# Performance work log

Hardware: AMD Instinct MI355X
Metric: run time of the kernel (lower is better)

Reference implementation:

```python
import jax, jax.numpy as jnp
import numpy as np


def setup_inputs() -> dict:
    key = jax.random.key(0)
    ks = jax.random.split(key, 8)
    B, I, H = 4096, 2048, 2048
    C = I + H
    s = 1.0 / np.sqrt(C)
    return {
        "x": jax.random.normal(ks[0], (B, I), jnp.float32),
        "h": jax.random.normal(ks[1], (B, H), jnp.float32),
        "W_update": jax.random.normal(ks[2], (H, C), jnp.float32) * s,
        "b_update": jax.random.normal(ks[3], (H,), jnp.float32) * s,
        "W_select": jax.random.normal(ks[4], (H, C), jnp.float32) * s,
        "b_select": jax.random.normal(ks[5], (H,), jnp.float32) * s,
        "W_predict": jax.random.normal(ks[6], (H, C), jnp.float32) * s,
        "b_predict": jax.random.normal(ks[7], (H,), jnp.float32) * s,
    }


def reference(x, h, W_update, b_update, W_select, b_select, W_predict, b_predict):
    # combined = [x, h]  -> [B, I+H]
    combined = jnp.concatenate([x, h], axis=1)
    to_update = jax.nn.sigmoid(combined @ W_update.T + b_update)  # [B, H]
    to_select = jax.nn.sigmoid(combined @ W_select.T + b_select)  # [B, H]
    updated = h * to_update
    new_combined = jnp.concatenate([x, updated], axis=1)
    predictions = jnp.tanh(new_combined @ W_predict.T + b_predict)
    selected = predictions * to_select
    h_new = h * (1.0 - to_select) + selected
    return h_new
```

## Files before the change

### kernel.cpp

```cpp
#include <hip/hip_runtime.h>
#include <stdint.h>

#define IDIM 2048
#define HDIM 2048
#define CDIM 4096
#define BDIM 4096
#define KDIM 4096

typedef float f32x4 __attribute__((ext_vector_type(4)));
typedef short s16x8 __attribute__((ext_vector_type(8)));
typedef unsigned short u16;
typedef u16 u16x8 __attribute__((ext_vector_type(8)));

__device__ __forceinline__ u16 f2bf(float f) {
    union { float f; uint32_t u; } v; v.f = f;
    uint32_t r = v.u + 0x7fffu + ((v.u >> 16) & 1u);
    return (u16)(r >> 16);
}

__device__ __forceinline__ void gload_lds16(const void* g, void* l) {
    __builtin_amdgcn_global_load_lds(
        (__attribute__((address_space(1))) void*)g,
        (__attribute__((address_space(3))) void*)l,
        16, 0, 0);
}

__global__ void cvt_bf16_kernel(const float* __restrict__ src, u16* __restrict__ dst,
                                int ngroups) {
    int i = blockIdx.x * blockDim.x + threadIdx.x;
    if (i >= ngroups) return;
    const float4* s4 = (const float4*)src;
    float4 v0 = s4[2 * i], v1 = s4[2 * i + 1];
    u16x8 o;
    o[0] = f2bf(v0.x); o[1] = f2bf(v0.y); o[2] = f2bf(v0.z); o[3] = f2bf(v0.w);
    o[4] = f2bf(v1.x); o[5] = f2bf(v1.y); o[6] = f2bf(v1.z); o[7] = f2bf(v1.w);
    ((u16x8*)dst)[i] = o;
}

__global__ void pack_combined_kernel(const float* __restrict__ x, const float* __restrict__ h,
                                     u16* __restrict__ comb, u16* __restrict__ newc) {
    int i = blockIdx.x * blockDim.x + threadIdx.x;
    if (i >= BDIM * (CDIM / 8)) return;
    int b = i >> 9;
    int c = (i & 511) * 8;
    const float* src = (c < IDIM) ? (x + (size_t)b * IDIM + c)
                                  : (h + (size_t)b * HDIM + (c - IDIM));
    float4 v0 = ((const float4*)src)[0], v1 = ((const float4*)src)[1];
    u16x8 o;
    o[0] = f2bf(v0.x); o[1] = f2bf(v0.y); o[2] = f2bf(v0.z); o[3] = f2bf(v0.w);
    o[4] = f2bf(v1.x); o[5] = f2bf(v1.y); o[6] = f2bf(v1.z); o[7] = f2bf(v1.w);
    *(u16x8*)(comb + (size_t)b * CDIM + c) = o;
    if (c < IDIM) *(u16x8*)(newc + (size_t)b * CDIM + c) = o;
}

template <int EP>
__global__ void gemm_bt(const u16* __restrict__ A, const u16* __restrict__ Bm,
                        const float* __restrict__ h,
                        const float* __restrict__ bias0, const float* __restrict__ bias1,
                        float* __restrict__ Sout, u16* __restrict__ newc) {
    constexpr int BM = 128, BK = 64;
    const int tid  = threadIdx.x;
    const int lane = tid & 63;
    const int wave = tid >> 6;
    const int wr = wave >> 1, wc = wave & 1;
    const int bm = blockIdx.y * BM;
    const int bn = blockIdx.x * BM;

    __shared__ __align__(16) u16 lA[BM * BK];
    __shared__ __align__(16) u16 lB[BM * BK];

    f32x4 acc[4][4] = {};

    const int srow = wave * 32 + (lane >> 3);
    const int sg   = (lane & 7) ^ (lane >> 3);

    auto stage = [&](int k0) {
        #pragma unroll
        for (int i = 0; i < 4; ++i) {
            const int r = srow + i * 8;
            gload_lds16(A  + (size_t)(bm + r) * KDIM + k0 + sg * 8,
                        &lA[(wave * 32 + i * 8) * 64]);
            gload_lds16(Bm + (size_t)(bn + r) * KDIM + k0 + sg * 8,
                        &lB[(wave * 32 + i * 8) * 64]);
        }
    };

    stage(0);
    constexpr int NT = KDIM / BK;
    for (int kt = 0; kt < NT; ++kt) {
        __syncthreads();
        #pragma unroll
        for (int ks = 0; ks < 2; ++ks) {
            s16x8 af[4], bfr[4];
            #pragma unroll
            for (int m = 0; m < 4; ++m) {
                const int row = wr * 64 + m * 16 + (lane & 15);
                const int j   = ks * 4 + (lane >> 4);
                af[m] = *(const s16x8*)&lA[row * 64 + ((j ^ (row & 7)) << 3)];
            }
            #pragma unroll
            for (int n = 0; n < 4; ++n) {
                const int row = wc * 64 + n * 16 + (lane & 15);
                const int j   = ks * 4 + (lane >> 4);
                bfr[n] = *(const s16x8*)&lB[row * 64 + ((j ^ (row & 7)) << 3)];
            }
            #pragma unroll
            for (int m = 0; m < 4; ++m)
                #pragma unroll
                for (int n = 0; n < 4; ++n)
                    acc[m][n] = __builtin_amdgcn_mfma_f32_16x16x32_bf16(
                        af[m], bfr[n], acc[m][n], 0, 0, 0);
        }
        __syncthreads();
        if (kt + 1 < NT) stage((kt + 1) * BK);
    }

    #pragma unroll
    for (int m = 0; m < 4; ++m) {
        const int r0 = bm + wr * 64 + m * 16 + ((lane >> 4) << 2);
        #pragma unroll
        for (int n = 0; n < 4; ++n) {
            const int col = bn + wc * 64 + n * 16 + (lane & 15);
            #pragma unroll
            for (int j = 0; j < 4; ++j) {
                const int r = r0 + j;
                const float v = acc[m][n][j];
                if (EP == 1) {
                    const float bv = (col < HDIM) ? bias0[col] : bias1[col - HDIM];
                    const float sgm = 1.0f / (1.0f + __expf(-(v + bv)));
                    if (col < HDIM) {
                        const float hv = h[(size_t)r * HDIM + col];
                        newc[(size_t)r * CDIM + IDIM + col] = f2bf(hv * sgm);
                    } else {
                        Sout[(size_t)r * HDIM + (col - HDIM)] = sgm;
                    }
                } else {
                    const float p  = tanhf(v + bias0[col]);
                    const size_t idx = (size_t)r * HDIM + col;
                    const float s  = Sout[idx];
                    const float hv = h[idx];
                    Sout[idx] = hv * (1.0f - s) + p * s;
                }
            }
        }
    }
}

extern "C" void kernel_launch(void* const* d_in, const int* in_sizes, int n_in,
                              void* d_out, int out_size, void* d_ws, size_t ws_size,
                              hipStream_t stream) {
    (void)in_sizes; (void)n_in; (void)out_size; (void)ws_size;
    const float* x  = (const float*)d_in[0];
    const float* h  = (const float*)d_in[1];
    const float* Wu = (const float*)d_in[2];
    const float* bu = (const float*)d_in[3];
    const float* Ws = (const float*)d_in[4];
    const float* bs = (const float*)d_in[5];
    const float* Wp = (const float*)d_in[6];
    const float* bp = (const float*)d_in[7];
    float* out = (float*)d_out;

    u16* comb  = (u16*)d_ws;
    u16* newc  = comb  + (size_t)BDIM * CDIM;
    u16* wpack = newc  + (size_t)BDIM * CDIM;
    u16* wpred = wpack + (size_t)2 * HDIM * CDIM;

    const int WG = 256;
    const int wgrp = (HDIM * CDIM) / 8;
    cvt_bf16_kernel<<<wgrp / WG, WG, 0, stream>>>(Wu, wpack, wgrp);
    cvt_bf16_kernel<<<wgrp / WG, WG, 0, stream>>>(Ws, wpack + (size_t)HDIM * CDIM, wgrp);
    cvt_bf16_kernel<<<wgrp / WG, WG, 0, stream>>>(Wp, wpred, wgrp);
    const int cgrp = (BDIM * CDIM) / 8;
    pack_combined_kernel<<<cgrp / WG, WG, 0, stream>>>(x, h, comb, newc);

    gemm_bt<1><<<dim3(CDIM / 128, BDIM / 128), 256, 0, stream>>>(
        comb, wpack, h, bu, bs, out, newc);
    gemm_bt<2><<<dim3(HDIM / 128, BDIM / 128), 256, 0, stream>>>(
        newc, wpred, h, bp, nullptr, out, nullptr);
}
```

Measured before the change: 296.4 us.

## Replace GEMM with 8-wave double-buffered ping-pong kernel using larger tiles

Replaces the 4-wave 128x128 single-buffer GEMM with an 8-wave kernel that uses 256-wide N tiles (256x256 or 128x256) and double-buffered LDS. Each K step is split into four MFMA phases interleaved with asynchronous global-to-LDS prefetch of the next tile, using explicit barriers, waitcnt and setprio. The aim is to overlap memory loads with matrix math and raise data reuse per block. It adds more LDS use, hand-tuned vmcnt counts that must match the issued loads, and fewer blocks for the second GEMM.

```diff
diff --git a/kernel.cpp b/kernel.cpp
--- a/kernel.cpp
+++ b/kernel.cpp
@@ -53,94 +53,156 @@
     if (c < IDIM) *(u16x8*)(newc + (size_t)b * CDIM + c) = o;
 }
 
-template <int EP>
-__global__ void gemm_bt(const u16* __restrict__ A, const u16* __restrict__ Bm,
-                        const float* __restrict__ h,
-                        const float* __restrict__ bias0, const float* __restrict__ bias1,
-                        float* __restrict__ Sout, u16* __restrict__ newc) {
-    constexpr int BM = 128, BK = 64;
+template <int BM, int EP>
+__global__ __launch_bounds__(512, 2) void gemm8p(
+        const u16* __restrict__ A, const u16* __restrict__ Bm,
+        const float* __restrict__ h,
+        const float* __restrict__ bias0, const float* __restrict__ bias1,
+        float* __restrict__ Sout, u16* __restrict__ newc) {
+    constexpr int MF_H = (BM == 256) ? 4 : 2;
+    constexpr int QMS  = (BM == 256) ? 128 : 32;
+    constexpr int NT   = KDIM / 64;
+
     const int tid  = threadIdx.x;
     const int lane = tid & 63;
     const int wave = tid >> 6;
-    const int wr = wave >> 1, wc = wave & 1;
+    const int wr = wave >> 2, wc = wave & 3;
     const int bm = blockIdx.y * BM;
-    const int bn = blockIdx.x * BM;
-
-    __shared__ __align__(16) u16 lA[BM * BK];
-    __shared__ __align__(16) u16 lB[BM * BK];
-
-    f32x4 acc[4][4] = {};
-
-    const int srow = wave * 32 + (lane >> 3);
-    const int sg   = (lane & 7) ^ (lane >> 3);
-
-    auto stage = [&](int k0) {
+    const int bn = blockIdx.x * 256;
+
+    __shared__ __align__(16) u16 lA[2][BM * 64];
+    __shared__ __align__(16) u16 lB[2][256 * 64];
+
+    f32x4 acc[2 * MF_H][4] = {};
+    s16x8 af[MF_H][2];
+    s16x8 bq[2][2][2];
+
+    const int srow = tid >> 3;
+    const int ssw  = ((tid & 7) ^ ((tid >> 3) & 7)) << 3;
+
+    auto stageA = [&](int nb, int c, int k0) {
+        gload_lds16(A + (size_t)(bm + c * 64 + srow) * KDIM + k0 + ssw,
+                    &lA[nb][(c * 64 + wave * 8) * 64]);
+    };
+    auto stageB = [&](int nb, int c, int k0) {
+        gload_lds16(Bm + (size_t)(bn + c * 64 + srow) * KDIM + k0 + ssw,
+                    &lB[nb][(c * 64 + wave * 8) * 64]);
+    };
+
+#define READ_A(QM)                                                              \
+    _Pragma("unroll") for (int fm = 0; fm < MF_H; ++fm) {                       \
+        const int row_ = wr * 64 + (QM) * QMS + fm * 16 + (lane & 15);          \
+        const int bo_ = row_ * 64; const int rx_ = row_ & 7;                    \
+        af[fm][0] = *(const s16x8*)&curA[bo_ + ((((lane >> 4)    ) ^ rx_) << 3)]; \
+        af[fm][1] = *(const s16x8*)&curA[bo_ + ((((lane >> 4) + 4) ^ rx_) << 3)]; \
+    }
+#define READ_B(QN)                                                              \
+    _Pragma("unroll") for (int nf = 0; nf < 2; ++nf) {                          \
+        const int row_ = wc * 32 + (QN) * 128 + nf * 16 + (lane & 15);          \
+        const int bo_ = row_ * 64; const int rx_ = row_ & 7;                    \
+        bq[QN][nf][0] = *(const s16x8*)&curB[bo_ + ((((lane >> 4)    ) ^ rx_) << 3)]; \
+        bq[QN][nf][1] = *(const s16x8*)&curB[bo_ + ((((lane >> 4) + 4) ^ rx_) << 3)]; \
+    }
+#define MFMA_QUAD(QM, QN)                                                       \
+    _Pragma("unroll") for (int ks = 0; ks < 2; ++ks)                            \
+    _Pragma("unroll") for (int fm = 0; fm < MF_H; ++fm)                         \
+    _Pragma("unroll") for (int nf = 0; nf < 2; ++nf)                            \
+        acc[(QM) * MF_H + fm][(QN) * 2 + nf] =                                  \
+            __builtin_amdgcn_mfma_f32_16x16x32_bf16(                            \
+                af[fm][ks], bq[QN][nf][ks], acc[(QM) * MF_H + fm][(QN) * 2 + nf], 0, 0, 0);
+#define PHASE_MID()                                                             \
+    __builtin_amdgcn_s_barrier();                                               \
+    asm volatile("s_waitcnt lgkmcnt(0)" ::: "memory");                          \
+    __builtin_amdgcn_sched_barrier(0);                                          \
+    __builtin_amdgcn_s_setprio(1);
+#define PHASE_END_NOWAIT()                                                      \
+    __builtin_amdgcn_s_setprio(0);                                              \
+    __builtin_amdgcn_s_barrier();
+#define PHASE_END_WAIT()                                                        \
+    __builtin_amdgcn_s_setprio(0);                                              \
+    if constexpr (BM == 256) { asm volatile("s_waitcnt vmcnt(4)" ::: "memory"); } \
+    else                     { asm volatile("s_waitcnt vmcnt(2)" ::: "memory"); } \
+    __builtin_amdgcn_s_barrier();
+
+    stageA(0, 0, 0); stageA(0, 1, 0);
+    stageB(0, 0, 0); stageB(0, 1, 0); stageB(0, 2, 0); stageB(0, 3, 0);
+    if constexpr (BM == 256) { stageA(0, 2, 0); stageA(0, 3, 0); }
+    if constexpr (BM == 256) { asm volatile("s_waitcnt vmcnt(4)" ::: "memory"); }
+    else                     { asm volatile("s_waitcnt vmcnt(2)" ::: "memory"); }
+    __builtin_amdgcn_s_barrier();
+
+    for (int kt = 0; kt < NT; ++kt) {
+        const u16* curA = lA[kt & 1];
+        const u16* curB = lB[kt & 1];
+        const int nb = (kt & 1) ^ 1;
+        const int kn = (kt + 1) * 64;
+        const bool pf = (kt + 1 < NT);
+
+        READ_A(0)
+        READ_B(0)
+        if (pf) { stageA(nb, 0, kn); stageA(nb, 1, kn); }
+        PHASE_MID();
+        MFMA_QUAD(0, 0);
+        PHASE_END_WAIT();
+
+        READ_B(1)
+        if (pf) { stageB(nb, 0, kn); stageB(nb, 1, kn); }
+        PHASE_MID();
+        MFMA_QUAD(0, 1);
+        if constexpr (BM == 256) { PHASE_END_WAIT(); }
+        else                     { PHASE_END_NOWAIT(); }
+
+        READ_A(1)
+        if (pf) { stageB(nb, 2, kn); stageB(nb, 3, kn); }
+        PHASE_MID();
+        MFMA_QUAD(1, 1);
+        PHASE_END_NOWAIT();
+
+        if constexpr (BM == 256) {
+            if (pf) { stageA(nb, 2, kn); stageA(nb, 3, kn); }
+        }
+        PHASE_MID();
+        MFMA_QUAD(1, 0);
+        PHASE_END_WAIT();
+    }
+
+#undef READ_A
+#undef READ_B
+#undef MFMA_QUAD
+#undef PHASE_MID
+#undef PHASE_END_NOWAIT
+#undef PHASE_END_WAIT
+
+    #pragma unroll
+    for (int qm = 0; qm < 2; ++qm)
+    #pragma unroll
+    for (int fm = 0; fm < MF_H; ++fm)
+    #pragma unroll
+    for (int qn = 0; qn < 2; ++qn)
+    #pragma unroll
+    for (int nf = 0; nf < 2; ++nf) {
+        const int r0  = bm + wr * 64 + qm * QMS + fm * 16 + ((lane >> 4) << 2);
+        const int col = bn + wc * 32 + qn * 128 + nf * 16 + (lane & 15);
+        const f32x4 a = acc[qm * MF_H + fm][qn * 2 + nf];
         #pragma unroll
-        for (int i = 0; i < 4; ++i) {
-            const int r = srow + i * 8;
-            gload_lds16(A  + (size_t)(bm + r) * KDIM + k0 + sg * 8,
-                        &lA[(wave * 32 + i * 8) * 64]);
-            gload_lds16(Bm + (size_t)(bn + r) * KDIM + k0 + sg * 8,
-                        &lB[(wave * 32 + i * 8) * 64]);
-        }
-    };
-
-    stage(0);
-    constexpr int NT = KDIM / BK;
-    for (int kt = 0; kt < NT; ++kt) {
-        __syncthreads();
-        #pragma unroll
-        for (int ks = 0; ks < 2; ++ks) {
-            s16x8 af[4], bfr[4];
-            #pragma unroll
-            for (int m = 0; m < 4; ++m) {
-                const int row = wr * 64 + m * 16 + (lane & 15);
-                const int j   = ks * 4 + (lane >> 4);
-                af[m] = *(const s16x8*)&lA[row * 64 + ((j ^ (row & 7)) << 3)];
-            }
-            #pragma unroll
-            for (int n = 0; n < 4; ++n) {
-                const int row = wc * 64 + n * 16 + (lane & 15);
-                const int j   = ks * 4 + (lane >> 4);
-                bfr[n] = *(const s16x8*)&lB[row * 64 + ((j ^ (row & 7)) << 3)];
-            }
-            #pragma unroll
-            for (int m = 0; m < 4; ++m)
-                #pragma unroll
-                for (int n = 0; n < 4; ++n)
-                    acc[m][n] = __builtin_amdgcn_mfma_f32_16x16x32_bf16(
-                        af[m], bfr[n], acc[m][n], 0, 0, 0);
-        }
-        __syncthreads();
-        if (kt + 1 < NT) stage((kt + 1) * BK);
-    }
-
-    #pragma unroll
-    for (int m = 0; m < 4; ++m) {
-        const int r0 = bm + wr * 64 + m * 16 + ((lane >> 4) << 2);
-        #pragma unroll
-        for (int n = 0; n < 4; ++n) {
-            const int col = bn + wc * 64 + n * 16 + (lane & 15);
-            #pragma unroll
-            for (int j = 0; j < 4; ++j) {
-                const int r = r0 + j;
-                const float v = acc[m][n][j];
-                if (EP == 1) {
-                    const float bv = (col < HDIM) ? bias0[col] : bias1[col - HDIM];
-                    const float sgm = 1.0f / (1.0f + __expf(-(v + bv)));
-                    if (col < HDIM) {
-                        const float hv = h[(size_t)r * HDIM + col];
-                        newc[(size_t)r * CDIM + IDIM + col] = f2bf(hv * sgm);
-                    } else {
-                        Sout[(size_t)r * HDIM + (col - HDIM)] = sgm;
-                    }
+        for (int j = 0; j < 4; ++j) {
+            const int r = r0 + j;
+            const float v = a[j];
+            if constexpr (EP == 1) {
+                const float bv = (col < HDIM) ? bias0[col] : bias1[col - HDIM];
+                const float sgm = 1.0f / (1.0f + __expf(-(v + bv)));
+                if (col < HDIM) {
+                    const float hv = h[(size_t)r * HDIM + col];
+                    newc[(size_t)r * CDIM + IDIM + col] = f2bf(hv * sgm);
                 } else {
-                    const float p  = tanhf(v + bias0[col]);
-                    const size_t idx = (size_t)r * HDIM + col;
-                    const float s  = Sout[idx];
-                    const float hv = h[idx];
-                    Sout[idx] = hv * (1.0f - s) + p * s;
+                    Sout[(size_t)r * HDIM + (col - HDIM)] = sgm;
                 }
+            } else {
+                const float p = tanhf(v + bias0[col]);
+                const size_t idx = (size_t)r * HDIM + col;
+                const float s = Sout[idx];
+                const float hv = h[idx];
+                Sout[idx] = hv * (1.0f - s) + p * s;
             }
         }
     }
@@ -173,8 +235,8 @@
     const int cgrp = (BDIM * CDIM) / 8;
     pack_combined_kernel<<<cgrp / WG, WG, 0, stream>>>(x, h, comb, newc);
 
-    gemm_bt<1><<<dim3(CDIM / 128, BDIM / 128), 256, 0, stream>>>(
+    gemm8p<256, 1><<<dim3(CDIM / 256, BDIM / 256), 512, 0, stream>>>(
         comb, wpack, h, bu, bs, out, newc);
-    gemm_bt<2><<<dim3(HDIM / 128, BDIM / 128), 256, 0, stream>>>(
+    gemm8p<128, 2><<<dim3(HDIM / 256, BDIM / 128), 512, 0, stream>>>(
         newc, wpred, h, bp, nullptr, out, nullptr);
 }
```

Measured after the change: 332.0 us. +12.0%, slower.

## Split K within each GEMM block across two wave groups with LDS reduction

Applied to the files above, without the earlier changes.

Each 128x128 output tile is now computed by 512 threads, split into two groups of four waves. The K tile doubles to 128, and each group handles half of it. After the main loop, the second group writes its partial accumulators to LDS and the first group adds them before running the fused epilogue. The aim is more waves per CU to hide latency and fewer barrier iterations, at the cost of 64KB of LDS per block (which limits occupancy), an extra reduction pass, and half the waves sitting idle during the epilogue.

```diff
diff --git a/kernel.cpp b/kernel.cpp
--- a/kernel.cpp
+++ b/kernel.cpp
@@ -54,39 +54,42 @@
 }
 
 template <int EP>
-__global__ void gemm_bt(const u16* __restrict__ A, const u16* __restrict__ Bm,
-                        const float* __restrict__ h,
-                        const float* __restrict__ bias0, const float* __restrict__ bias1,
-                        float* __restrict__ Sout, u16* __restrict__ newc) {
-    constexpr int BM = 128, BK = 64;
+__global__ __launch_bounds__(512, 4) void gemm_sk(
+        const u16* __restrict__ A, const u16* __restrict__ Bm,
+        const float* __restrict__ h,
+        const float* __restrict__ bias0, const float* __restrict__ bias1,
+        float* __restrict__ Sout, u16* __restrict__ newc) {
+    constexpr int BK = 128, NT = KDIM / BK;
     const int tid  = threadIdx.x;
     const int lane = tid & 63;
     const int wave = tid >> 6;
-    const int wr = wave >> 1, wc = wave & 1;
-    const int bm = blockIdx.y * BM;
-    const int bn = blockIdx.x * BM;
-
-    __shared__ __align__(16) u16 lA[BM * BK];
-    __shared__ __align__(16) u16 lB[BM * BK];
+    const int kg = wave >> 2;
+    const int wq = wave & 3;
+    const int wr = wq >> 1, wc = wq & 1;
+    const int bm = blockIdx.y * 128;
+    const int bn = blockIdx.x * 128;
+
+    __shared__ __align__(16) u16 smem[2 * 128 * 128];
+    u16* lA = smem;
+    u16* lB = smem + 128 * 128;
 
     f32x4 acc[4][4] = {};
 
-    const int srow = wave * 32 + (lane >> 3);
-    const int sg   = (lane & 7) ^ (lane >> 3);
+    const int srow  = tid >> 4;
+    const int sslot = ((tid & 15) ^ (srow & 15)) << 3;
 
     auto stage = [&](int k0) {
         #pragma unroll
-        for (int i = 0; i < 4; ++i) {
-            const int r = srow + i * 8;
-            gload_lds16(A  + (size_t)(bm + r) * KDIM + k0 + sg * 8,
-                        &lA[(wave * 32 + i * 8) * 64]);
-            gload_lds16(Bm + (size_t)(bn + r) * KDIM + k0 + sg * 8,
-                        &lB[(wave * 32 + i * 8) * 64]);
-        }
+        for (int c = 0; c < 4; ++c)
+            gload_lds16(A + (size_t)(bm + c * 32 + srow) * KDIM + k0 + sslot,
+                        &lA[(c * 32 + wave * 4) * 128]);
+        #pragma unroll
+        for (int c = 0; c < 4; ++c)
+            gload_lds16(Bm + (size_t)(bn + c * 32 + srow) * KDIM + k0 + sslot,
+                        &lB[(c * 32 + wave * 4) * 128]);
     };
 
     stage(0);
-    constexpr int NT = KDIM / BK;
     for (int kt = 0; kt < NT; ++kt) {
         __syncthreads();
         #pragma unroll
@@ -95,14 +98,14 @@
             #pragma unroll
             for (int m = 0; m < 4; ++m) {
                 const int row = wr * 64 + m * 16 + (lane & 15);
-                const int j   = ks * 4 + (lane >> 4);
-                af[m] = *(const s16x8*)&lA[row * 64 + ((j ^ (row & 7)) << 3)];
+                const int j   = kg * 8 + ks * 4 + (lane >> 4);
+                af[m] = *(const s16x8*)&lA[row * 128 + ((j ^ (row & 15)) << 3)];
             }
             #pragma unroll
             for (int n = 0; n < 4; ++n) {
                 const int row = wc * 64 + n * 16 + (lane & 15);
-                const int j   = ks * 4 + (lane >> 4);
-                bfr[n] = *(const s16x8*)&lB[row * 64 + ((j ^ (row & 7)) << 3)];
+                const int j   = kg * 8 + ks * 4 + (lane >> 4);
+                bfr[n] = *(const s16x8*)&lB[row * 128 + ((j ^ (row & 15)) << 3)];
             }
             #pragma unroll
             for (int m = 0; m < 4; ++m)
@@ -115,31 +118,48 @@
         if (kt + 1 < NT) stage((kt + 1) * BK);
     }
 
-    #pragma unroll
-    for (int m = 0; m < 4; ++m) {
-        const int r0 = bm + wr * 64 + m * 16 + ((lane >> 4) << 2);
-        #pragma unroll
-        for (int n = 0; n < 4; ++n) {
-            const int col = bn + wc * 64 + n * 16 + (lane & 15);
-            #pragma unroll
-            for (int j = 0; j < 4; ++j) {
-                const int r = r0 + j;
-                const float v = acc[m][n][j];
-                if (EP == 1) {
-                    const float bv = (col < HDIM) ? bias0[col] : bias1[col - HDIM];
-                    const float sgm = 1.0f / (1.0f + __expf(-(v + bv)));
-                    if (col < HDIM) {
-                        const float hv = h[(size_t)r * HDIM + col];
-                        newc[(size_t)r * CDIM + IDIM + col] = f2bf(hv * sgm);
+    f32x4* red = (f32x4*)smem;
+    if (kg == 1) {
+        #pragma unroll
+        for (int m = 0; m < 4; ++m)
+            #pragma unroll
+            for (int n = 0; n < 4; ++n)
+                red[wq * 1024 + (m * 4 + n) * 64 + lane] = acc[m][n];
+    }
+    __syncthreads();
+    if (kg == 0) {
+        #pragma unroll
+        for (int m = 0; m < 4; ++m)
+            #pragma unroll
+            for (int n = 0; n < 4; ++n)
+                acc[m][n] += red[wq * 1024 + (m * 4 + n) * 64 + lane];
+
+        #pragma unroll
+        for (int m = 0; m < 4; ++m) {
+            const int r0 = bm + wr * 64 + m * 16 + ((lane >> 4) << 2);
+            #pragma unroll
+            for (int n = 0; n < 4; ++n) {
+                const int col = bn + wc * 64 + n * 16 + (lane & 15);
+                #pragma unroll
+                for (int j = 0; j < 4; ++j) {
+                    const int r = r0 + j;
+                    const float v = acc[m][n][j];
+                    if constexpr (EP == 1) {
+                        const float bv = (col < HDIM) ? bias0[col] : bias1[col - HDIM];
+                        const float sgm = 1.0f / (1.0f + __expf(-(v + bv)));
+                        if (col < HDIM) {
+                            const float hv = h[(size_t)r * HDIM + col];
+                            newc[(size_t)r * CDIM + IDIM + col] = f2bf(hv * sgm);
+                        } else {
+                            Sout[(size_t)r * HDIM + (col - HDIM)] = sgm;
+                        }
                     } else {
-                        Sout[(size_t)r * HDIM + (col - HDIM)] = sgm;
+                        const float p = tanhf(v + bias0[col]);
+                        const size_t idx = (size_t)r * HDIM + col;
+                        const float s  = Sout[idx];
+                        const float hv = h[idx];
+                        Sout[idx] = hv * (1.0f - s) + p * s;
                     }
-                } else {
-                    const float p  = tanhf(v + bias0[col]);
-                    const size_t idx = (size_t)r * HDIM + col;
-                    const float s  = Sout[idx];
-                    const float hv = h[idx];
-                    Sout[idx] = hv * (1.0f - s) + p * s;
                 }
             }
         }
@@ -173,8 +193,8 @@
     const int cgrp = (BDIM * CDIM) / 8;
     pack_combined_kernel<<<cgrp / WG, WG, 0, stream>>>(x, h, comb, newc);
 
-    gemm_bt<1><<<dim3(CDIM / 128, BDIM / 128), 256, 0, stream>>>(
+    gemm_sk<1><<<dim3(CDIM / 128, BDIM / 128), 512, 0, stream>>>(
         comb, wpack, h, bu, bs, out, newc);
-    gemm_bt<2><<<dim3(HDIM / 128, BDIM / 128), 256, 0, stream>>>(
+    gemm_sk<2><<<dim3(HDIM / 128, BDIM / 128), 512, 0, stream>>>(
         newc, wpred, h, bp, nullptr, out, nullptr);
 }
```

Result: slower. 311.2 us (+5.0%).
